# Kernel tuning notes

Hardware: AMD Instinct MI355X
Metric: run time of the kernel (lower is better)

The kernel has to match this reference:

```python
import jax, jax.numpy as jnp
import numpy as np

N_SU = 8
DATA_DIM = N_SU * N_SU - 1  # 63
BATCH = 1048576


def _gell_mann(n):
    """Generalized Gell-Mann matrices of su(n), Tr(L_a L_b) = 2 delta_ab."""
    mats = []
    for j in range(n):
        for k in range(j + 1, n):
            m = np.zeros((n, n), dtype=np.complex128); m[j, k] = 1.0; m[k, j] = 1.0
            mats.append(m)
            m = np.zeros((n, n), dtype=np.complex128); m[j, k] = -1.0j; m[k, j] = 1.0j
            mats.append(m)
    for l in range(1, n):
        m = np.zeros((n, n), dtype=np.complex128)
        c = np.sqrt(2.0 / (l * (l + 1)))
        for j in range(l):
            m[j, j] = c
        m[l, l] = -l * c
        mats.append(m)
    return np.stack(mats)


def _structure_const(n):
    """f_abc = Tr([L_a,L_b]L_c)/(4i), d_abc = Tr({L_a,L_b}L_c)/4 (both real)."""
    L = _gell_mann(n)                                  # (D, n, n)
    P = np.einsum('aij,bjk->abik', L, L)               # L_a L_b
    comm = P - P.transpose(1, 0, 2, 3)
    anti = P + P.transpose(1, 0, 2, 3)
    f = (np.einsum('abik,cki->abc', comm, L) / 4.0j).real
    d = (np.einsum('abik,cki->abc', anti, L) / 4.0).real
    return f.astype(np.float32), d.astype(np.float32)

F_CONST, D_CONST = _structure_const(N_SU)              # (D, D, D) each, compile-time constants
TRI = np.stack(np.triu_indices(DATA_DIM, 0))           # incl. diagonal
TRI1 = np.stack(np.triu_indices(DATA_DIM, 1))          # strict upper


def setup_inputs() -> dict:
    key = jax.random.key(0)
    k1, k2, k3, k4, k5 = jax.random.split(key, 5)
    D = DATA_DIM
    return {
        'x': jax.random.normal(k1, (BATCH, D), dtype=jnp.float32),
        'r_x': jax.random.uniform(k2, (D * (D + 1) // 2,), dtype=jnp.float32),
        'r_y': jax.random.uniform(k3, (D * (D - 1) // 2,), dtype=jnp.float32),
        'N': jax.random.uniform(k4, (1,), dtype=jnp.float32),
        'omega': jax.random.uniform(k5, (D,), dtype=jnp.float32),
    }


def _forward(x, r_x, r_y, N, omega):
    f = jnp.asarray(F_CONST)
    d = jnp.asarray(D_CONST)
    D = DATA_DIM
    # NOTE: faithful to the torch source, where `v_x = v_y = torch.zeros(...)`
    # aliases ONE tensor: r_y overwrites r_x on the strict upper triangle and
    # v_x is v_y, which makes c_im exactly zero.
    v = jnp.zeros((D, D), dtype=x.dtype)
    v = v.at[TRI[0], TRI[1]].set(r_x)
    v = v.at[TRI1[0], TRI1[1]].set(r_y)
    v_x = v
    v_y = v
    c_re = v_x.T @ v_x + v_y.T @ v_y                   # einsum('ki,kj->ij', v, v) x2
    c_re = c_re / jnp.trace(c_re)
    c_im = v_x.T @ v_y - v_y.T @ v_x                   # exactly zero (aliasing)
    c_re = N * c_re

    # Precompute the small (D,D) superoperator coefficient matrices once, then
    # apply them to the batch with plain matmuls (bn,mn->bm).
    A1 = jnp.einsum('mjk,ij->mik', f, c_re)
    M_re1 = jnp.einsum('mik,nik->mn', A1, f)           # 'mjk,nik,ij->mn'
    A2 = jnp.einsum('mik,ij->mjk', f, c_re)
    M_re2 = jnp.einsum('mjk,njk->mn', A2, f)           # 'mik,njk,ij->mn'
    B1 = jnp.einsum('mjk,ij->mik', f, c_im)
    M_im1 = jnp.einsum('mik,nik->mn', B1, d)
    B2 = jnp.einsum('mik,ij->mjk', f, c_im)
    M_im2 = jnp.einsum('mjk,njk->mn', B2, d)
    M = -2.0 * M_re1 - 2.0 * M_re2 - 2.0 * M_im1 + 2.0 * M_im2

    d_super_x = x @ M.T                                 # (B, D)
    H = 8.0 * jnp.einsum('kij,k->ij', f, omega)
    h_commutator_x = x @ H.T                            # 'kij,k,bj->bi'
    tr_id = -8.0 * jnp.einsum('imj,ij->m', f, c_im)     # (D,), zero here

    S_x = h_commutator_x + d_super_x
    T_x = x + tr_id
    L_x = S_x + T_x
    return x + 0.01 * L_x


def reference(x, r_x, r_y, N, omega):
    return _forward(x, r_x, r_y, N, omega)
```

## Files before the change

### kernel.cpp

```cpp
#include <hip/hip_runtime.h>
#include <hip/hip_bf16.h>

#define DD 63
#define DD2 (DD * DD)
#define NSU 8

typedef __attribute__((ext_vector_type(8))) short short8;
typedef __attribute__((ext_vector_type(4))) float f32x4;

__device__ float  g_F[DD2 * DD];
__device__ float  g_B[DD * DD2];
__device__ float  g_cc[DD2];
__device__ float  g_scale;
__device__ unsigned short g_Gb[64 * 64];

__device__ __forceinline__ unsigned short f2bf(float f) {
    union { float f; unsigned u; } v; v.f = f;
    unsigned r = v.u + 0x7FFFu + ((v.u >> 16) & 1u);
    return (unsigned short)(r >> 16);
}

__device__ __forceinline__ void fill_L(int a, float (*re)[NSU], float (*im)[NSU]) {
    if (a < 56) {
        int p = a >> 1;
        int j = 0, rem = p;
        while (rem >= 7 - j) { rem -= 7 - j; ++j; }
        int k = j + 1 + rem;
        if ((a & 1) == 0) { re[j][k] = 1.f; re[k][j] = 1.f; }
        else             { im[j][k] = -1.f; im[k][j] = 1.f; }
    } else {
        int l = a - 55;
        float c = sqrtf(2.f / (float)(l * (l + 1)));
        for (int j = 0; j < l; ++j) re[j][j] = c;
        re[l][l] = -(float)l * c;
    }
}

__global__ __launch_bounds__(256) void setup_kernel(const float* __restrict__ r_x,
                                                    const float* __restrict__ r_y,
                                                    const float* __restrict__ Np) {
    const int t = threadIdx.x;
    if (blockIdx.x < DD) {
        const int a = blockIdx.x;
        __shared__ float Ar[NSU][NSU], Ai[NSU][NSU];
        __shared__ float Br[4][NSU][NSU], Bi[4][NSU][NSU];
        __shared__ float Cr[4][NSU][NSU], Ci[4][NSU][NSU];
        const int w = t >> 6, lane = t & 63;
        const int r = lane >> 3, c = lane & 7;
        if (t < 64) { Ar[r][c] = 0.f; Ai[r][c] = 0.f; }
        __syncthreads();
        if (t == 0) fill_L(a, Ar, Ai);
        __syncthreads();
        for (int rb = 0; rb < 16; ++rb) {
            const int b = rb * 4 + w;
            const bool act = (b < DD);
            if (act) { Br[w][r][c] = 0.f; Bi[w][r][c] = 0.f; }
            __syncthreads();
            if (act && lane == 0) fill_L(b, Br[w], Bi[w]);
            __syncthreads();
            if (act) {
                float pr = 0.f, pi = 0.f, qr = 0.f, qi = 0.f;
                #pragma unroll
                for (int k = 0; k < NSU; ++k) {
                    pr += Ar[r][k] * Br[w][k][c] - Ai[r][k] * Bi[w][k][c];
                    pi += Ar[r][k] * Bi[w][k][c] + Ai[r][k] * Br[w][k][c];
                    qr += Br[w][r][k] * Ar[k][c] - Bi[w][r][k] * Ai[k][c];
                    qi += Br[w][r][k] * Ai[k][c] + Bi[w][r][k] * Ar[k][c];
                }
                Cr[w][r][c] = pr - qr;
                Ci[w][r][c] = pi - qi;
            }
            __syncthreads();
            if (act && lane < DD) {
                float im;
                if (lane < 56) {
                    int p = lane >> 1;
                    int j = 0, rem = p;
                    while (rem >= 7 - j) { rem -= 7 - j; ++j; }
                    int k = j + 1 + rem;
                    if ((lane & 1) == 0) im = Ci[w][j][k] + Ci[w][k][j];
                    else                 im = Cr[w][j][k] - Cr[w][k][j];
                } else {
                    int l = lane - 55;
                    float cd = sqrtf(2.f / (float)(l * (l + 1)));
                    float s = 0.f;
                    for (int j = 0; j < l; ++j) s += Ci[w][j][j];
                    im = cd * s - (float)l * cd * Ci[w][l][l];
                }
                g_F[(a * DD + b) * DD + lane] = 0.25f * im;
            }
            __syncthreads();
        }
    } else {
        __shared__ float v[DD2];
        __shared__ float ccs[DD2];
        for (int idx = t; idx < DD2; idx += 256) {
            int i = idx / DD, j = idx % DD;
            float val = 0.f;
            if (j > i)       val = r_y[62 * i - (i * (i - 1)) / 2 + (j - i - 1)];
            else if (j == i) val = r_x[63 * i - (i * (i - 1)) / 2];
            v[idx] = val;
        }
        __syncthreads();
        for (int idx = t; idx < DD2; idx += 256) {
            int i = idx / DD, j = idx % DD;
            float s = 0.f;
            for (int k = 0; k < DD; ++k) s = fmaf(v[k * DD + i], v[k * DD + j], s);
            ccs[idx] = s;
            g_cc[idx] = s;
        }
        __syncthreads();
        if (t == 0) {
            float tr = 0.f;
            for (int i = 0; i < DD; ++i) tr += ccs[i * DD + i];
            g_scale = Np[0] / tr;
        }
    }
}

__global__ __launch_bounds__(256) void buildB_kernel() {
    __shared__ float scc[DD2];
    __shared__ float sf[DD2];
    const int t = threadIdx.x;
    const int n = blockIdx.x;
    for (int idx = t; idx < DD2; idx += 256) {
        scc[idx] = g_cc[idx];
        sf[idx]  = g_F[n * DD2 + idx];
    }
    __syncthreads();
    for (int idx = t; idx < DD2; idx += 256) {
        const int j = idx / DD, k = idx % DD;
        float s = 0.f;
        for (int i = 0; i < DD; ++i) s = fmaf(scc[i * DD + j], sf[i * DD + k], s);
        g_B[n * DD2 + idx] = s;
    }
}

__global__ __launch_bounds__(64) void buildKt_kernel(const float* __restrict__ omega) {
    const int m = blockIdx.x >> 6;
    const int n = blockIdx.x & 63;
    const int lane = threadIdx.x;
    if (m >= DD || n >= DD) {
        if (lane == 0) g_Gb[m * 64 + n] = 0;
        return;
    }
    const float* __restrict__ Fm = g_F + m * DD2;
    const float* __restrict__ Bn = g_B + n * DD2;
    float p = 0.f;
    for (int idx = lane; idx < DD2; idx += 64) p = fmaf(Fm[idx], Bn[idx], p);
    float h = (lane < DD) ? g_F[lane * DD2 + m * DD + n] * omega[lane] : 0.f;
    #pragma unroll
    for (int off = 32; off > 0; off >>= 1) {
        p += __shfl_down(p, off);
        h += __shfl_down(h, off);
    }
    if (lane == 0)
        g_Gb[m * 64 + n] = f2bf(0.01f * (-4.f * g_scale * p + 8.f * h)
                                + ((m == n) ? 1.01f : 0.f));
}

__global__ __launch_bounds__(256) void apply_kernel(const float* __restrict__ x,
                                                    float* __restrict__ out,
                                                    int ntiles, int nwaves) {
    const int t = threadIdx.x;
    const int w = t >> 6, lane = t & 63;
    const int mrow = lane & 15;
    const int q = lane >> 4;
    const int wave_id = blockIdx.x * 4 + w;

    const short8* __restrict__ gG = (const short8*)g_Gb;
    short8 bfrag[2][4];
    #pragma unroll
    for (int kt = 0; kt < 2; ++kt)
        #pragma unroll
        for (int nt = 0; nt < 4; ++nt)
            bfrag[kt][nt] = gG[(nt * 16 + mrow) * 8 + kt * 4 + q];

    for (int tile = wave_id; tile < ntiles; tile += nwaves) {
        const size_t tbase = (size_t)tile * (16 * DD);
        const float* __restrict__ rp = x + tbase + mrow * DD;

        float va[2][8];
        #pragma unroll
        for (int kt = 0; kt < 2; ++kt)
            #pragma unroll
            for (int j = 0; j < 8; ++j) {
                int k = kt * 32 + q * 8 + j;
                if (kt == 1 && j == 7) k = (k == 63) ? 62 : k;
                va[kt][j] = rp[k];
            }
        short8 af[2];
        #pragma unroll
        for (int kt = 0; kt < 2; ++kt)
            #pragma unroll
            for (int j = 0; j < 8; ++j) {
                __hip_bfloat16 h = __float2bfloat16(va[kt][j]);
                af[kt][j] = *reinterpret_cast<short*>(&h);
            }

        f32x4 acc[4] = {{0.f,0.f,0.f,0.f},{0.f,0.f,0.f,0.f},
                        {0.f,0.f,0.f,0.f},{0.f,0.f,0.f,0.f}};
        #pragma unroll
        for (int nt = 0; nt < 4; ++nt) {
            acc[nt] = __builtin_amdgcn_mfma_f32_16x16x32_bf16(af[0], bfrag[0][nt], acc[nt], 0, 0, 0);
            acc[nt] = __builtin_amdgcn_mfma_f32_16x16x32_bf16(af[1], bfrag[1][nt], acc[nt], 0, 0, 0);
        }

        #pragma unroll
        for (int nt = 0; nt < 4; ++nt) {
            const int ocol = nt * 16 + mrow;
            if (ocol < DD) {
                #pragma unroll
                for (int r = 0; r < 4; ++r)
                    out[tbase + (q * 4 + r) * DD + ocol] = acc[nt][r];
            }
        }
    }
}

extern "C" void kernel_launch(void* const* d_in, const int* in_sizes, int n_in,
                              void* d_out, int out_size, void* d_ws, size_t ws_size,
                              hipStream_t stream) {
    const float* x     = (const float*)d_in[0];
    const float* r_x   = (const float*)d_in[1];
    const float* r_y   = (const float*)d_in[2];
    const float* Np    = (const float*)d_in[3];
    const float* omega = (const float*)d_in[4];
    float* out = (float*)d_out;

    const int rows = in_sizes[0] / DD;
    const int ntiles = rows / 16;
    const int ablocks = 2048;
    const int nwaves = ablocks * 4;

    setup_kernel<<<DD + 1, 256, 0, stream>>>(r_x, r_y, Np);
    buildB_kernel<<<DD, 256, 0, stream>>>();
    buildKt_kernel<<<64 * 64, 64, 0, stream>>>(omega);
    apply_kernel<<<ablocks, 256, 0, stream>>>(x, out, ntiles, nwaves);
}
```

Measured before the change: 210.5 us.

## Stage x tiles through swizzled LDS with coalesced float4 IO and prefetch; merge setup kernels

The apply kernel now loads each 16-row tile of x with coalesced float4 global loads into a per-wave XOR-swizzled LDS slab. It reads MFMA A-fragments from that slab, prefetches the next tile into registers, and writes outputs back through LDS as coalesced float4 stores. This replaces strided scalar row loads and scattered scalar stores. Separately, the cc/B/G coefficient build is fused into one kernel per column, which drops one launch and the global g_B/g_cc round trips, but each block now recomputes cc redundantly.

```diff
diff --git a/kernel.cpp b/kernel.cpp
--- a/kernel.cpp
+++ b/kernel.cpp
@@ -9,9 +9,6 @@
 typedef __attribute__((ext_vector_type(4))) float f32x4;
 
 __device__ float  g_F[DD2 * DD];
-__device__ float  g_B[DD * DD2];
-__device__ float  g_cc[DD2];
-__device__ float  g_scale;
 __device__ unsigned short g_Gb[64 * 64];
 
 __device__ __forceinline__ unsigned short f2bf(float f) {
@@ -36,137 +33,134 @@
     }
 }
 
-__global__ __launch_bounds__(256) void setup_kernel(const float* __restrict__ r_x,
-                                                    const float* __restrict__ r_y,
-                                                    const float* __restrict__ Np) {
+__global__ __launch_bounds__(256) void setup_f_kernel() {
     const int t = threadIdx.x;
-    if (blockIdx.x < DD) {
-        const int a = blockIdx.x;
-        __shared__ float Ar[NSU][NSU], Ai[NSU][NSU];
-        __shared__ float Br[4][NSU][NSU], Bi[4][NSU][NSU];
-        __shared__ float Cr[4][NSU][NSU], Ci[4][NSU][NSU];
-        const int w = t >> 6, lane = t & 63;
-        const int r = lane >> 3, c = lane & 7;
-        if (t < 64) { Ar[r][c] = 0.f; Ai[r][c] = 0.f; }
-        __syncthreads();
-        if (t == 0) fill_L(a, Ar, Ai);
-        __syncthreads();
-        for (int rb = 0; rb < 16; ++rb) {
-            const int b = rb * 4 + w;
-            const bool act = (b < DD);
-            if (act) { Br[w][r][c] = 0.f; Bi[w][r][c] = 0.f; }
-            __syncthreads();
-            if (act && lane == 0) fill_L(b, Br[w], Bi[w]);
-            __syncthreads();
-            if (act) {
-                float pr = 0.f, pi = 0.f, qr = 0.f, qi = 0.f;
-                #pragma unroll
-                for (int k = 0; k < NSU; ++k) {
-                    pr += Ar[r][k] * Br[w][k][c] - Ai[r][k] * Bi[w][k][c];
-                    pi += Ar[r][k] * Bi[w][k][c] + Ai[r][k] * Br[w][k][c];
-                    qr += Br[w][r][k] * Ar[k][c] - Bi[w][r][k] * Ai[k][c];
-                    qi += Br[w][r][k] * Ai[k][c] + Bi[w][r][k] * Ar[k][c];
-                }
-                Cr[w][r][c] = pr - qr;
-                Ci[w][r][c] = pi - qi;
-            }
-            __syncthreads();
-            if (act && lane < DD) {
-                float im;
-                if (lane < 56) {
-                    int p = lane >> 1;
-                    int j = 0, rem = p;
-                    while (rem >= 7 - j) { rem -= 7 - j; ++j; }
-                    int k = j + 1 + rem;
-                    if ((lane & 1) == 0) im = Ci[w][j][k] + Ci[w][k][j];
-                    else                 im = Cr[w][j][k] - Cr[w][k][j];
-                } else {
-                    int l = lane - 55;
-                    float cd = sqrtf(2.f / (float)(l * (l + 1)));
-                    float s = 0.f;
-                    for (int j = 0; j < l; ++j) s += Ci[w][j][j];
-                    im = cd * s - (float)l * cd * Ci[w][l][l];
-                }
-                g_F[(a * DD + b) * DD + lane] = 0.25f * im;
-            }
-            __syncthreads();
-        }
-    } else {
-        __shared__ float v[DD2];
-        __shared__ float ccs[DD2];
-        for (int idx = t; idx < DD2; idx += 256) {
-            int i = idx / DD, j = idx % DD;
-            float val = 0.f;
-            if (j > i)       val = r_y[62 * i - (i * (i - 1)) / 2 + (j - i - 1)];
-            else if (j == i) val = r_x[63 * i - (i * (i - 1)) / 2];
-            v[idx] = val;
-        }
-        __syncthreads();
-        for (int idx = t; idx < DD2; idx += 256) {
-            int i = idx / DD, j = idx % DD;
-            float s = 0.f;
-            for (int k = 0; k < DD; ++k) s = fmaf(v[k * DD + i], v[k * DD + j], s);
-            ccs[idx] = s;
-            g_cc[idx] = s;
-        }
-        __syncthreads();
-        if (t == 0) {
-            float tr = 0.f;
-            for (int i = 0; i < DD; ++i) tr += ccs[i * DD + i];
-            g_scale = Np[0] / tr;
-        }
-    }
-}
-
-__global__ __launch_bounds__(256) void buildB_kernel() {
-    __shared__ float scc[DD2];
+    const int a = blockIdx.x;
+    __shared__ float Ar[NSU][NSU], Ai[NSU][NSU];
+    __shared__ float Br[4][NSU][NSU], Bi[4][NSU][NSU];
+    __shared__ float Cr[4][NSU][NSU], Ci[4][NSU][NSU];
+    const int w = t >> 6, lane = t & 63;
+    const int r = lane >> 3, c = lane & 7;
+    if (t < 64) { Ar[r][c] = 0.f; Ai[r][c] = 0.f; }
+    __syncthreads();
+    if (t == 0) fill_L(a, Ar, Ai);
+    __syncthreads();
+    for (int rb = 0; rb < 16; ++rb) {
+        const int b = rb * 4 + w;
+        const bool act = (b < DD);
+        if (act) { Br[w][r][c] = 0.f; Bi[w][r][c] = 0.f; }
+        __syncthreads();
+        if (act && lane == 0) fill_L(b, Br[w], Bi[w]);
+        __syncthreads();
+        if (act) {
+            float pr = 0.f, pi = 0.f, qr = 0.f, qi = 0.f;
+            #pragma unroll
+            for (int k = 0; k < NSU; ++k) {
+                pr += Ar[r][k] * Br[w][k][c] - Ai[r][k] * Bi[w][k][c];
+                pi += Ar[r][k] * Bi[w][k][c] + Ai[r][k] * Br[w][k][c];
+                qr += Br[w][r][k] * Ar[k][c] - Bi[w][r][k] * Ai[k][c];
+                qi += Br[w][r][k] * Ai[k][c] + Bi[w][r][k] * Ar[k][c];
+            }
+            Cr[w][r][c] = pr - qr;
+            Ci[w][r][c] = pi - qi;
+        }
+        __syncthreads();
+        if (act && lane < DD) {
+            float im;
+            if (lane < 56) {
+                int p = lane >> 1;
+                int j = 0, rem = p;
+                while (rem >= 7 - j) { rem -= 7 - j; ++j; }
+                int k = j + 1 + rem;
+                if ((lane & 1) == 0) im = Ci[w][j][k] + Ci[w][k][j];
+                else                 im = Cr[w][j][k] - Cr[w][k][j];
+            } else {
+                int l = lane - 55;
+                float cd = sqrtf(2.f / (float)(l * (l + 1)));
+                float s = 0.f;
+                for (int j = 0; j < l; ++j) s += Ci[w][j][j];
+                im = cd * s - (float)l * cd * Ci[w][l][l];
+            }
+            g_F[(a * DD + b) * DD + lane] = 0.25f * im;
+        }
+        __syncthreads();
+    }
+}
+
+__global__ __launch_bounds__(256) void buildG_kernel(const float* __restrict__ r_x,
+                                                     const float* __restrict__ r_y,
+                                                     const float* __restrict__ Np,
+                                                     const float* __restrict__ omega) {
+    __shared__ float v[DD2];
+    __shared__ float cc[DD2];
     __shared__ float sf[DD2];
+    __shared__ float Bs[DD2];
+    __shared__ float s_scale;
     const int t = threadIdx.x;
     const int n = blockIdx.x;
+
     for (int idx = t; idx < DD2; idx += 256) {
-        scc[idx] = g_cc[idx];
-        sf[idx]  = g_F[n * DD2 + idx];
+        sf[idx] = g_F[n * DD2 + idx];
+        int i = idx / DD, j = idx - i * DD;
+        float val = 0.f;
+        if (j > i)       val = r_y[62 * i - (i * (i - 1)) / 2 + (j - i - 1)];
+        else if (j == i) val = r_x[63 * i - (i * (i - 1)) / 2];
+        v[idx] = val;
     }
     __syncthreads();
     for (int idx = t; idx < DD2; idx += 256) {
-        const int j = idx / DD, k = idx % DD;
+        int i = idx / DD, j = idx - i * DD;
         float s = 0.f;
-        for (int i = 0; i < DD; ++i) s = fmaf(scc[i * DD + j], sf[i * DD + k], s);
-        g_B[n * DD2 + idx] = s;
-    }
-}
-
-__global__ __launch_bounds__(64) void buildKt_kernel(const float* __restrict__ omega) {
-    const int m = blockIdx.x >> 6;
-    const int n = blockIdx.x & 63;
-    const int lane = threadIdx.x;
-    if (m >= DD || n >= DD) {
-        if (lane == 0) g_Gb[m * 64 + n] = 0;
-        return;
-    }
-    const float* __restrict__ Fm = g_F + m * DD2;
-    const float* __restrict__ Bn = g_B + n * DD2;
-    float p = 0.f;
-    for (int idx = lane; idx < DD2; idx += 64) p = fmaf(Fm[idx], Bn[idx], p);
-    float h = (lane < DD) ? g_F[lane * DD2 + m * DD + n] * omega[lane] : 0.f;
-    #pragma unroll
-    for (int off = 32; off > 0; off >>= 1) {
-        p += __shfl_down(p, off);
-        h += __shfl_down(h, off);
-    }
-    if (lane == 0)
-        g_Gb[m * 64 + n] = f2bf(0.01f * (-4.f * g_scale * p + 8.f * h)
-                                + ((m == n) ? 1.01f : 0.f));
+        for (int k = 0; k < DD; ++k) s = fmaf(v[k * DD + i], v[k * DD + j], s);
+        cc[idx] = s;
+    }
+    __syncthreads();
+    if (t == 0) {
+        float tr = 0.f;
+        for (int i = 0; i < DD; ++i) tr += cc[i * DD + i];
+        s_scale = Np[0] / tr;
+    }
+    __syncthreads();
+    for (int idx = t; idx < DD2; idx += 256) {
+        int j = idx / DD, k = idx - j * DD;
+        float s = 0.f;
+        for (int i = 0; i < DD; ++i) s = fmaf(cc[i * DD + j], sf[i * DD + k], s);
+        Bs[idx] = s;
+    }
+    __syncthreads();
+
+    const int w = t >> 6, lane = t & 63;
+    const float sc = s_scale;
+    for (int r = 0; r < 16; ++r) {
+        const int m = r * 4 + w;
+        if (m >= DD) continue;
+        const float* __restrict__ Fm = g_F + m * DD2;
+        float p = 0.f;
+        for (int idx = lane; idx < DD2; idx += 64) p = fmaf(Fm[idx], Bs[idx], p);
+        float h = (lane < DD) ? g_F[lane * DD2 + m * DD + n] * omega[lane] : 0.f;
+        #pragma unroll
+        for (int off = 32; off > 0; off >>= 1) {
+            p += __shfl_down(p, off);
+            h += __shfl_down(h, off);
+        }
+        if (lane == 0)
+            g_Gb[m * 64 + n] = f2bf(0.01f * (-4.f * sc * p + 8.f * h)
+                                    + ((m == n) ? 1.01f : 0.f));
+    }
+    if (n == 0 && t < 64) {
+        g_Gb[63 * 64 + t] = 0;
+        g_Gb[t * 64 + 63] = 0;
+    }
 }
 
 __global__ __launch_bounds__(256) void apply_kernel(const float* __restrict__ x,
                                                     float* __restrict__ out,
                                                     int ntiles, int nwaves) {
+    __shared__ float slab[4][16 * 64];
     const int t = threadIdx.x;
     const int w = t >> 6, lane = t & 63;
-    const int mrow = lane & 15;
-    const int q = lane >> 4;
-    const int wave_id = blockIdx.x * 4 + w;
+    const int mrow = lane & 15, q = lane >> 4;
+    float* __restrict__ S = slab[w];
 
     const short8* __restrict__ gG = (const short8*)g_Gb;
     short8 bfrag[2][4];
@@ -176,19 +170,58 @@
         for (int nt = 0; nt < 4; ++nt)
             bfrag[kt][nt] = gG[(nt * 16 + mrow) * 8 + kt * 4 + q];
 
-    for (int tile = wave_id; tile < ntiles; tile += nwaves) {
-        const size_t tbase = (size_t)tile * (16 * DD);
-        const float* __restrict__ rp = x + tbase + mrow * DD;
+    if (lane < 16) S[lane * 64 + (((15 ^ lane) << 2) | 3)] = 0.f;
+
+    int soff[4][4];
+    #pragma unroll
+    for (int i = 0; i < 4; ++i) {
+        const int f = i * 64 + lane;
+        #pragma unroll
+        for (int j = 0; j < 4; ++j) {
+            const int e = 4 * f + j;
+            const int r = e / 63, c = e - r * 63;
+            soff[i][j] = r * 64 + ((((c >> 2) ^ r) << 2) | (c & 3));
+        }
+    }
+    const bool act3 = (lane < 60);
+
+    int tile = blockIdx.x * 4 + w;
+    if (tile >= ntiles) return;
+
+    float4 ld[4];
+    {
+        const float4* __restrict__ gp = (const float4*)(x + (size_t)tile * (16 * DD));
+        ld[0] = gp[lane]; ld[1] = gp[lane + 64]; ld[2] = gp[lane + 128];
+        if (act3) ld[3] = gp[lane + 192];
+    }
+
+    while (true) {
+        #pragma unroll
+        for (int i = 0; i < 3; ++i) {
+            S[soff[i][0]] = ld[i].x; S[soff[i][1]] = ld[i].y;
+            S[soff[i][2]] = ld[i].z; S[soff[i][3]] = ld[i].w;
+        }
+        if (act3) {
+            S[soff[3][0]] = ld[3].x; S[soff[3][1]] = ld[3].y;
+            S[soff[3][2]] = ld[3].z; S[soff[3][3]] = ld[3].w;
+        }
+        const size_t tb = (size_t)tile * (16 * DD);
+        const int next = tile + nwaves;
 
         float va[2][8];
         #pragma unroll
-        for (int kt = 0; kt < 2; ++kt)
-            #pragma unroll
-            for (int j = 0; j < 8; ++j) {
-                int k = kt * 32 + q * 8 + j;
-                if (kt == 1 && j == 7) k = (k == 63) ? 62 : k;
-                va[kt][j] = rp[k];
-            }
+        for (int kt = 0; kt < 2; ++kt) {
+            const int c0 = 8 * kt + 2 * q;
+            *(float4*)&va[kt][0] = *(const float4*)&S[mrow * 64 + (((c0    ) ^ mrow) << 2)];
+            *(float4*)&va[kt][4] = *(const float4*)&S[mrow * 64 + (((c0 + 1) ^ mrow) << 2)];
+        }
+
+        if (next < ntiles) {
+            const float4* __restrict__ gp = (const float4*)(x + (size_t)next * (16 * DD));
+            ld[0] = gp[lane]; ld[1] = gp[lane + 64]; ld[2] = gp[lane + 128];
+            if (act3) ld[3] = gp[lane + 192];
+        }
+
         short8 af[2];
         #pragma unroll
         for (int kt = 0; kt < 2; ++kt)
@@ -211,10 +244,29 @@
             const int ocol = nt * 16 + mrow;
             if (ocol < DD) {
                 #pragma unroll
-                for (int r = 0; r < 4; ++r)
-                    out[tbase + (q * 4 + r) * DD + ocol] = acc[nt][r];
-            }
-        }
+                for (int r = 0; r < 4; ++r) {
+                    const int orow = q * 4 + r;
+                    S[orow * 64 + ((((ocol >> 2) ^ orow) << 2) | (ocol & 3))] = acc[nt][r];
+                }
+            }
+        }
+
+        #pragma unroll
+        for (int i = 0; i < 3; ++i) {
+            float4 o;
+            o.x = S[soff[i][0]]; o.y = S[soff[i][1]];
+            o.z = S[soff[i][2]]; o.w = S[soff[i][3]];
+            ((float4*)(out + tb))[i * 64 + lane] = o;
+        }
+        if (act3) {
+            float4 o;
+            o.x = S[soff[3][0]]; o.y = S[soff[3][1]];
+            o.z = S[soff[3][2]]; o.w = S[soff[3][3]];
+            ((float4*)(out + tb))[192 + lane] = o;
+        }
+
+        if (next >= ntiles) break;
+        tile = next;
     }
 }
 
@@ -233,8 +285,7 @@
     const int ablocks = 2048;
     const int nwaves = ablocks * 4;
 
-    setup_kernel<<<DD + 1, 256, 0, stream>>>(r_x, r_y, Np);
-    buildB_kernel<<<DD, 256, 0, stream>>>();
-    buildKt_kernel<<<64 * 64, 64, 0, stream>>>(omega);
+    setup_f_kernel<<<DD, 256, 0, stream>>>();
+    buildG_kernel<<<DD, 256, 0, stream>>>(r_x, r_y, Np, omega);
     apply_kernel<<<ablocks, 256, 0, stream>>>(x, out, ntiles, nwaves);
 }
```

Result: slower. 364.1 us (+73.0%).
